# Kernel optimization log

Measured on AMD Instinct MI355X. Metric: run time of the kernel, lower is better.

## Reference

```python
import jax, jax.numpy as jnp
import numpy as np

B, S, D, H, DH = 2, 2048, 2048, 16, 128


def _rope(t, cos, sin):
    # t: [b,s,h,dh]; pairs are consecutive elements (view(..., -1, 2) in torch)
    te = t[..., 0::2]
    to = t[..., 1::2]
    re = te * cos - to * sin
    im = te * sin + to * cos
    return jnp.stack([re, im], axis=-1).reshape(t.shape)


def setup_inputs() -> dict:
    key = jax.random.key(0)
    ks = jax.random.split(key, 5)
    inv = 1.0 / np.sqrt(D)
    x = jax.random.normal(ks[0], (B, S, D), dtype=jnp.float32)
    # standard RoPE angle table -> cos/sin of shape [1,S,1,DH//2]
    pos = jnp.arange(S, dtype=jnp.float32)[:, None]
    freqs = 1.0 / (10000.0 ** (jnp.arange(0, DH, 2, dtype=jnp.float32) / DH))
    ang = pos * freqs[None, :]
    rope_cos = jnp.cos(ang)[None, :, None, :]
    rope_sin = jnp.sin(ang)[None, :, None, :]
    Wq = jax.random.normal(ks[1], (D, D), dtype=jnp.float32) * inv
    Wk = jax.random.normal(ks[2], (D, D), dtype=jnp.float32) * inv
    Wv = jax.random.normal(ks[3], (D, D), dtype=jnp.float32) * inv
    Wo = jax.random.normal(ks[4], (D, D), dtype=jnp.float32) * inv
    return {"x": x, "rope_cos": rope_cos, "rope_sin": rope_sin,
            "Wq": Wq, "Wk": Wk, "Wv": Wv, "Wo": Wo}


def reference(x, rope_cos, rope_sin, Wq, Wk, Wv, Wo):
    b, s, d = x.shape
    scale = DH ** (-0.5)
    # nn.Linear(bias=False): y = x @ W.T
    q = (x @ Wq.T).reshape(b, s, H, DH)
    k = (x @ Wk.T).reshape(b, s, H, DH)
    v = (x @ Wv.T).reshape(b, s, H, DH)
    q = _rope(q, rope_cos[:, :s], rope_sin[:, :s])
    k = _rope(k, rope_cos[:, :s], rope_sin[:, :s])
    q = q.transpose(0, 2, 1, 3)  # bhsd
    k = k.transpose(0, 2, 1, 3)
    v = v.transpose(0, 2, 1, 3)
    # full scores needed for softmax normalizer
    scores = jnp.einsum('bhqd,bhkd->bhqk', q, k) * scale
    lse = jax.nn.logsumexp(scores, axis=-1)  # [b,h,s]
    # torch.einsum('bhss,bhsd->bhsd', softmax(scores), v) takes the DIAGONAL
    # of the softmax matrix and scales v elementwise. Replicate exactly:
    diag = jnp.einsum('bhsd,bhsd->bhs', q, k) * scale  # scores[b,h,s,s]
    w = jnp.exp(diag - lse)  # softmax(scores)[b,h,s,s]
    out = w[..., None] * v  # [b,h,s,dh]
    out = out.transpose(0, 2, 1, 3).reshape(b, s, d)
    return out @ Wo.T
```

## Files before the change

kernel.cpp:

```cpp
#include <hip/hip_runtime.h>

#define B_  2
#define S_  2048
#define D_  2048
#define H_  16
#define DH_ 128
#define M_  (B_ * S_)

typedef __bf16 bf16;
typedef __bf16 bf16x2 __attribute__((ext_vector_type(2)));
typedef __bf16 bf16x4 __attribute__((ext_vector_type(4)));
typedef __bf16 bf16x8 __attribute__((ext_vector_type(8)));
typedef float  f32x4  __attribute__((ext_vector_type(4)));

static constexpr float kScale = 0.08838834764831845f;

__device__ __forceinline__ void async16(const void* g, void* l) {
  __builtin_amdgcn_global_load_lds(
      (const __attribute__((address_space(1))) void*)g,
      (__attribute__((address_space(3))) void*)l, 16, 0, 0);
}

__global__ void cvt_bf16(const float* __restrict__ s, bf16* __restrict__ d) {
  int i = (blockIdx.x * 256 + threadIdx.x) * 4;
  float4 v = *(const float4*)(s + i);
  bf16x4 o = {(bf16)v.x, (bf16)v.y, (bf16)v.z, (bf16)v.w};
  *(bf16x4*)(d + i) = o;
}

__global__ __launch_bounds__(256, 2) void gemm_qkv(
    const bf16* __restrict__ A, const bf16* __restrict__ Bm,
    bf16* __restrict__ qb, bf16* __restrict__ kb, bf16* __restrict__ vb) {
  __shared__ alignas(16) bf16 As[128 * 32];
  __shared__ alignas(16) bf16 Bs[128 * 32];
  const int tid = threadIdx.x;
  const int lane = tid & 63, wv = tid >> 6;
  const int quad = lane >> 4, c16 = lane & 15;
  const int wm = (wv >> 1) * 64, wn = (wv & 1) * 64;
  const int m0 = blockIdx.y * 128, n0 = blockIdx.x * 128;

  const bf16* ag = A  + (size_t)(m0 + (tid >> 2)) * D_ + (tid & 3) * 8;
  const bf16* bg = Bm + (size_t)(n0 + (tid >> 2)) * D_ + (tid & 3) * 8;
  char* asl = (char*)As + tid * 16;
  char* bsl = (char*)Bs + tid * 16;

  f32x4 acc[4][4] = {};
  for (int k0 = 0; k0 < D_; k0 += 32) {
    __syncthreads();
    async16(ag + k0,            asl);
    async16(ag + k0 + 64 * D_,  asl + 4096);
    async16(bg + k0,            bsl);
    async16(bg + k0 + 64 * D_,  bsl + 4096);
    __syncthreads();
    bf16x8 af[4], bfr[4];
#pragma unroll
    for (int i = 0; i < 4; ++i)
      af[i] = *(const bf16x8*)(As + (wm + i * 16 + c16) * 32 + quad * 8);
#pragma unroll
    for (int j = 0; j < 4; ++j)
      bfr[j] = *(const bf16x8*)(Bs + (wn + j * 16 + c16) * 32 + quad * 8);
#pragma unroll
    for (int i = 0; i < 4; ++i)
#pragma unroll
      for (int j = 0; j < 4; ++j)
        acc[i][j] = __builtin_amdgcn_mfma_f32_16x16x32_bf16(af[i], bfr[j], acc[i][j], 0, 0, 0);
  }

#pragma unroll
  for (int i = 0; i < 4; ++i)
#pragma unroll
    for (int j = 0; j < 4; ++j)
#pragma unroll
      for (int r = 0; r < 4; ++r) {
        int gm = m0 + wm + i * 16 + quad * 4 + r;
        int gn = n0 + wn + j * 16 + c16;
        float v = acc[i][j][r];
        int b = gm >> 11, s = gm & 2047;
        if (gn < 2048) {
          int h = gn >> 7, d = gn & 127;
          qb[(size_t)((b * 16 + h) * 2048 + s) * 128 + d] = (bf16)v;
        } else if (gn < 4096) {
          int h = (gn - 2048) >> 7, d = gn & 127;
          kb[(size_t)((b * 16 + h) * 2048 + s) * 128 + d] = (bf16)v;
        } else {
          vb[(size_t)gm * 2048 + (gn - 4096)] = (bf16)v;
        }
      }
}

__global__ void rope_kernel(bf16* __restrict__ q, bf16* __restrict__ k,
                            const float* __restrict__ cb, const float* __restrict__ sb) {
  int p  = blockIdx.x * 256 + threadIdx.x;
  int si = p & (S_ * 64 - 1);
  float c = cb[si], sn = sb[si];
  bf16x2* qp = (bf16x2*)q + p;
  bf16x2 qv = *qp;
  float te = (float)qv[0], to = (float)qv[1];
  bf16x2 oq = {(bf16)((te * c - to * sn) * kScale), (bf16)((te * sn + to * c) * kScale)};
  *qp = oq;
  bf16x2* kp = (bf16x2*)k + p;
  bf16x2 kv = *kp;
  te = (float)kv[0]; to = (float)kv[1];
  bf16x2 ok = {(bf16)(te * c - to * sn), (bf16)(te * sn + to * c)};
  *kp = ok;
}

__global__ __launch_bounds__(256, 2) void score_lse(
    const bf16* __restrict__ qb, const bf16* __restrict__ kb,
    float* __restrict__ lse, float* __restrict__ diag) {
  __shared__ alignas(16) bf16 Qs[4 * 128 * 32];
  __shared__ alignas(16) bf16 Ks[4 * 128 * 32];
  const int tid = threadIdx.x;
  const int lane = tid & 63, wv = tid >> 6;
  const int quad = lane >> 4, c16 = lane & 15;
  const int wm = wv * 32;
  const int bh = blockIdx.y;
  const int m0 = blockIdx.x * 128;
  const bf16* Q  = qb + (size_t)bh * (S_ * DH_);
  const bf16* Kp = kb + (size_t)bh * (S_ * DH_);

  const bf16* qg = Q + (size_t)(m0 + (tid >> 2)) * DH_ + (tid & 3) * 8;
  char* ql = (char*)Qs + tid * 16;
#pragma unroll
  for (int kt = 0; kt < 4; ++kt) {
    async16(qg + kt * 32,             ql + kt * 8192);
    async16(qg + kt * 32 + 64 * DH_,  ql + kt * 8192 + 4096);
  }

  const bf16* kg = Kp + (size_t)(tid >> 2) * DH_ + (tid & 3) * 8;
  char* kl = (char*)Ks + tid * 16;

  float sums[8] = {0.f, 0.f, 0.f, 0.f, 0.f, 0.f, 0.f, 0.f};

  for (int n0 = 0; n0 < S_; n0 += 128) {
    __syncthreads();
#pragma unroll
    for (int kt = 0; kt < 4; ++kt) {
      async16(kg + (size_t)n0 * DH_ + kt * 32,            kl + kt * 8192);
      async16(kg + (size_t)(n0 + 64) * DH_ + kt * 32,     kl + kt * 8192 + 4096);
    }
    __syncthreads();
    f32x4 acc[2][8] = {};
#pragma unroll
    for (int kt = 0; kt < 4; ++kt) {
      bf16x8 a[2], b[8];
#pragma unroll
      for (int i = 0; i < 2; ++i)
        a[i] = *(const bf16x8*)(Qs + kt * 4096 + (wm + i * 16 + c16) * 32 + quad * 8);
#pragma unroll
      for (int j = 0; j < 8; ++j)
        b[j] = *(const bf16x8*)(Ks + kt * 4096 + (j * 16 + c16) * 32 + quad * 8);
#pragma unroll
      for (int i = 0; i < 2; ++i)
#pragma unroll
        for (int j = 0; j < 8; ++j)
          acc[i][j] = __builtin_amdgcn_mfma_f32_16x16x32_bf16(a[i], b[j], acc[i][j], 0, 0, 0);
    }
#pragma unroll
    for (int i = 0; i < 2; ++i)
#pragma unroll
      for (int j = 0; j < 8; ++j)
#pragma unroll
        for (int r = 0; r < 4; ++r) {
          float sc = acc[i][j][r];
          int row = wm + i * 16 + quad * 4 + r;
          int col = j * 16 + c16;
          sums[i * 4 + r] += __expf(sc);
          if (n0 + col == m0 + row)
            diag[bh * S_ + m0 + row] = sc;
        }
  }

#pragma unroll
  for (int t = 0; t < 8; ++t) {
    float s = sums[t];
    s += __shfl_xor(s, 1);
    s += __shfl_xor(s, 2);
    s += __shfl_xor(s, 4);
    s += __shfl_xor(s, 8);
    if (c16 == 0) {
      int i = t >> 2, r = t & 3;
      lse[bh * S_ + m0 + wm + i * 16 + quad * 4 + r] = __logf(s);
    }
  }
}

__global__ void wv_mul(const bf16* __restrict__ vb, const float* __restrict__ lse,
                       const float* __restrict__ diag, bf16* __restrict__ t) {
  int u = blockIdx.x * 256 + threadIdx.x;
  int e = u * 8;
  int m = e >> 11;
  int c = e & 2047;
  int g = ((m >> 11) * 16 + (c >> 7)) * 2048 + (m & 2047);
  float w = __expf(diag[g] - lse[g]);
  bf16x8 v = ((const bf16x8*)vb)[u];
  bf16x8 o;
#pragma unroll
  for (int r = 0; r < 8; ++r) o[r] = (bf16)((float)v[r] * w);
  ((bf16x8*)t)[u] = o;
}

__global__ __launch_bounds__(256, 2) void gemm_out(
    const bf16* __restrict__ A, const bf16* __restrict__ Bm, float* __restrict__ C) {
  __shared__ alignas(16) bf16 As[128 * 32];
  __shared__ alignas(16) bf16 Bs[128 * 32];
  const int tid = threadIdx.x;
  const int lane = tid & 63, wv = tid >> 6;
  const int quad = lane >> 4, c16 = lane & 15;
  const int wm = (wv >> 1) * 64, wn = (wv & 1) * 64;
  const int m0 = blockIdx.y * 128, n0 = blockIdx.x * 128;

  const bf16* ag = A  + (size_t)(m0 + (tid >> 2)) * D_ + (tid & 3) * 8;
  const bf16* bg = Bm + (size_t)(n0 + (tid >> 2)) * D_ + (tid & 3) * 8;
  char* asl = (char*)As + tid * 16;
  char* bsl = (char*)Bs + tid * 16;

  f32x4 acc[4][4] = {};
  for (int k0 = 0; k0 < D_; k0 += 32) {
    __syncthreads();
    async16(ag + k0,            asl);
    async16(ag + k0 + 64 * D_,  asl + 4096);
    async16(bg + k0,            bsl);
    async16(bg + k0 + 64 * D_,  bsl + 4096);
    __syncthreads();
    bf16x8 af[4], bfr[4];
#pragma unroll
    for (int i = 0; i < 4; ++i)
      af[i] = *(const bf16x8*)(As + (wm + i * 16 + c16) * 32 + quad * 8);
#pragma unroll
    for (int j = 0; j < 4; ++j)
      bfr[j] = *(const bf16x8*)(Bs + (wn + j * 16 + c16) * 32 + quad * 8);
#pragma unroll
    for (int i = 0; i < 4; ++i)
#pragma unroll
      for (int j = 0; j < 4; ++j)
        acc[i][j] = __builtin_amdgcn_mfma_f32_16x16x32_bf16(af[i], bfr[j], acc[i][j], 0, 0, 0);
  }
#pragma unroll
  for (int i = 0; i < 4; ++i)
#pragma unroll
    for (int j = 0; j < 4; ++j)
#pragma unroll
      for (int r = 0; r < 4; ++r) {
        int gm = m0 + wm + i * 16 + quad * 4 + r;
        int gn = n0 + wn + j * 16 + c16;
        C[(size_t)gm * D_ + gn] = acc[i][j][r];
      }
}

extern "C" void kernel_launch(void* const* d_in, const int* in_sizes, int n_in,
                              void* d_out, int out_size, void* d_ws, size_t ws_size,
                              hipStream_t stream) {
  (void)in_sizes; (void)n_in; (void)out_size; (void)ws_size;
  const float* x  = (const float*)d_in[0];
  const float* rc = (const float*)d_in[1];
  const float* rs = (const float*)d_in[2];
  const float* Wq = (const float*)d_in[3];
  const float* Wk = (const float*)d_in[4];
  const float* Wv = (const float*)d_in[5];
  const float* Wo = (const float*)d_in[6];

  char* ws = (char*)d_ws;
  bf16* xb   = (bf16*)ws;
  bf16* wqkv = (bf16*)(ws + 16777216);
  bf16* wob  = (bf16*)(ws + 16777216 + 25165824);
  bf16* qb   = (bf16*)(ws + 16777216 + 25165824 + 8388608);
  bf16* kb   = qb + 8388608;
  bf16* vb   = kb + 8388608;
  float* lse = (float*)(vb + 8388608);
  float* dia = lse + 65536;

  cvt_bf16<<<8192, 256, 0, stream>>>(x,  xb);
  cvt_bf16<<<4096, 256, 0, stream>>>(Wq, wqkv);
  cvt_bf16<<<4096, 256, 0, stream>>>(Wk, wqkv + 4194304);
  cvt_bf16<<<4096, 256, 0, stream>>>(Wv, wqkv + 8388608);
  cvt_bf16<<<4096, 256, 0, stream>>>(Wo, wob);

  gemm_qkv<<<dim3(48, 32), 256, 0, stream>>>(xb, wqkv, qb, kb, vb);
  rope_kernel<<<16384, 256, 0, stream>>>(qb, kb, rc, rs);
  score_lse<<<dim3(16, 32), 256, 0, stream>>>(qb, kb, lse, dia);
  wv_mul<<<4096, 256, 0, stream>>>(vb, lse, dia, xb );
  gemm_out<<<dim3(16, 32), 256, 0, stream>>>(xb, wob, (float*)d_out);
}
```

Before: 396.2 us.

## Fuse RoPE into QKV GEMM epilogue and switch softmax to exp2

Removes the separate RoPE kernel by applying the rotation in the QKV GEMM epilogue, using lane shuffles to pair adjacent columns and writing bf16x2 stores. Folds log2(e) into the Q scale so the score kernel can use hardware exp2/log2. Diagonal extraction now runs only on the diagonal tile, and the output GEMM writes float2 stores. The cost is extra cos/sin loads and shuffles in the GEMM epilogue, plus slightly different rounding because RoPE is applied to the fp32 accumulator.

```diff
diff --git a/kernel.cpp b/kernel.cpp
--- a/kernel.cpp
+++ b/kernel.cpp
@@ -13,7 +13,10 @@
 typedef __bf16 bf16x8 __attribute__((ext_vector_type(8)));
 typedef float  f32x4  __attribute__((ext_vector_type(4)));
 
-static constexpr float kScale = 0.08838834764831845f;
+#define EXP2F(x) __builtin_amdgcn_exp2f(x)
+#define LOG2F(x) __builtin_amdgcn_logf(x)
+
+static constexpr float kQScale = 0.08838834764831845f * 1.4426950408889634f;
 
 __device__ __forceinline__ void async16(const void* g, void* l) {
   __builtin_amdgcn_global_load_lds(
@@ -30,6 +33,7 @@
 
 __global__ __launch_bounds__(256, 2) void gemm_qkv(
     const bf16* __restrict__ A, const bf16* __restrict__ Bm,
+    const float* __restrict__ rc, const float* __restrict__ rs,
     bf16* __restrict__ qb, bf16* __restrict__ kb, bf16* __restrict__ vb) {
   __shared__ alignas(16) bf16 As[128 * 32];
   __shared__ alignas(16) bf16 Bs[128 * 32];
@@ -66,43 +70,53 @@
         acc[i][j] = __builtin_amdgcn_mfma_f32_16x16x32_bf16(af[i], bfr[j], acc[i][j], 0, 0, 0);
   }
 
-#pragma unroll
-  for (int i = 0; i < 4; ++i)
-#pragma unroll
-    for (int j = 0; j < 4; ++j)
-#pragma unroll
-      for (int r = 0; r < 4; ++r) {
-        int gm = m0 + wm + i * 16 + quad * 4 + r;
-        int gn = n0 + wn + j * 16 + c16;
-        float v = acc[i][j][r];
-        int b = gm >> 11, s = gm & 2047;
-        if (gn < 2048) {
-          int h = gn >> 7, d = gn & 127;
-          qb[(size_t)((b * 16 + h) * 2048 + s) * 128 + d] = (bf16)v;
-        } else if (gn < 4096) {
-          int h = (gn - 2048) >> 7, d = gn & 127;
-          kb[(size_t)((b * 16 + h) * 2048 + s) * 128 + d] = (bf16)v;
-        } else {
-          vb[(size_t)gm * 2048 + (gn - 4096)] = (bf16)v;
+  if (n0 < 4096) {
+    bf16* dst = (n0 < 2048) ? qb : kb;
+    const float sc = (n0 < 2048) ? kQScale : 1.0f;
+#pragma unroll
+    for (int i = 0; i < 4; ++i) {
+      const int gmi = m0 + wm + i * 16 + quad * 4;
+#pragma unroll
+      for (int j = 0; j < 4; ++j) {
+        const int gn = n0 + wn + j * 16 + c16;
+        const int h = (gn >> 7) & 15;
+        const int d = gn & 127;
+#pragma unroll
+        for (int r = 0; r < 4; ++r) {
+          float v = acc[i][j][r];
+          float p = __shfl_xor(v, 1);
+          const int gm = gmi + r;
+          const int b = gm >> 11, s = gm & 2047;
+          const int si = s * 64 + (d >> 1);
+          float c = rc[si], sn = rs[si];
+          float re = (v * c - p * sn) * sc;
+          float im = (v * sn + p * c) * sc;
+          if (!(lane & 1)) {
+            bf16x2 o = {(bf16)re, (bf16)im};
+            *(bf16x2*)(dst + ((size_t)((b * 16 + h) * 2048 + s) * 128 + d)) = o;
+          }
         }
       }
-}
-
-__global__ void rope_kernel(bf16* __restrict__ q, bf16* __restrict__ k,
-                            const float* __restrict__ cb, const float* __restrict__ sb) {
-  int p  = blockIdx.x * 256 + threadIdx.x;
-  int si = p & (S_ * 64 - 1);
-  float c = cb[si], sn = sb[si];
-  bf16x2* qp = (bf16x2*)q + p;
-  bf16x2 qv = *qp;
-  float te = (float)qv[0], to = (float)qv[1];
-  bf16x2 oq = {(bf16)((te * c - to * sn) * kScale), (bf16)((te * sn + to * c) * kScale)};
-  *qp = oq;
-  bf16x2* kp = (bf16x2*)k + p;
-  bf16x2 kv = *kp;
-  te = (float)kv[0]; to = (float)kv[1];
-  bf16x2 ok = {(bf16)(te * c - to * sn), (bf16)(te * sn + to * c)};
-  *kp = ok;
+    }
+  } else {
+#pragma unroll
+    for (int i = 0; i < 4; ++i) {
+      const int gmi = m0 + wm + i * 16 + quad * 4;
+#pragma unroll
+      for (int j = 0; j < 4; ++j) {
+        const int gn = n0 + wn + j * 16 + c16 - 4096;
+#pragma unroll
+        for (int r = 0; r < 4; ++r) {
+          float v = acc[i][j][r];
+          float p = __shfl_xor(v, 1);
+          if (!(lane & 1)) {
+            bf16x2 o = {(bf16)v, (bf16)p};
+            *(bf16x2*)(vb + (size_t)(gmi + r) * 2048 + gn) = o;
+          }
+        }
+      }
+    }
+  }
 }
 
 __global__ __launch_bounds__(256, 2) void score_lse(
@@ -156,19 +170,24 @@
         for (int j = 0; j < 8; ++j)
           acc[i][j] = __builtin_amdgcn_mfma_f32_16x16x32_bf16(a[i], b[j], acc[i][j], 0, 0, 0);
     }
+    if (n0 == m0) {
+#pragma unroll
+      for (int i = 0; i < 2; ++i)
+#pragma unroll
+        for (int r = 0; r < 4; ++r) {
+          if (c16 == quad * 4 + r) {
+            int row = wm + i * 16 + quad * 4 + r;
+            diag[bh * S_ + m0 + row] = acc[i][2 * wv + i][r];
+          }
+        }
+    }
 #pragma unroll
     for (int i = 0; i < 2; ++i)
 #pragma unroll
       for (int j = 0; j < 8; ++j)
 #pragma unroll
-        for (int r = 0; r < 4; ++r) {
-          float sc = acc[i][j][r];
-          int row = wm + i * 16 + quad * 4 + r;
-          int col = j * 16 + c16;
-          sums[i * 4 + r] += __expf(sc);
-          if (n0 + col == m0 + row)
-            diag[bh * S_ + m0 + row] = sc;
-        }
+        for (int r = 0; r < 4; ++r)
+          sums[i * 4 + r] += EXP2F(acc[i][j][r]);
   }
 
 #pragma unroll
@@ -180,7 +199,7 @@
     s += __shfl_xor(s, 8);
     if (c16 == 0) {
       int i = t >> 2, r = t & 3;
-      lse[bh * S_ + m0 + wm + i * 16 + quad * 4 + r] = __logf(s);
+      lse[bh * S_ + m0 + wm + i * 16 + quad * 4 + r] = LOG2F(s);
     }
   }
 }
@@ -192,7 +211,7 @@
   int m = e >> 11;
   int c = e & 2047;
   int g = ((m >> 11) * 16 + (c >> 7)) * 2048 + (m & 2047);
-  float w = __expf(diag[g] - lse[g]);
+  float w = EXP2F(diag[g] - lse[g]);
   bf16x8 v = ((const bf16x8*)vb)[u];
   bf16x8 o;
 #pragma unroll
@@ -242,9 +261,14 @@
     for (int j = 0; j < 4; ++j)
 #pragma unroll
       for (int r = 0; r < 4; ++r) {
-        int gm = m0 + wm + i * 16 + quad * 4 + r;
-        int gn = n0 + wn + j * 16 + c16;
-        C[(size_t)gm * D_ + gn] = acc[i][j][r];
+        float v = acc[i][j][r];
+        float p = __shfl_xor(v, 1);
+        if (!(lane & 1)) {
+          int gm = m0 + wm + i * 16 + quad * 4 + r;
+          int gn = n0 + wn + j * 16 + c16;
+          float2 o = {v, p};
+          *(float2*)(C + (size_t)gm * D_ + gn) = o;
+        }
       }
 }
 
@@ -276,8 +300,7 @@
   cvt_bf16<<<4096, 256, 0, stream>>>(Wv, wqkv + 8388608);
   cvt_bf16<<<4096, 256, 0, stream>>>(Wo, wob);
 
-  gemm_qkv<<<dim3(48, 32), 256, 0, stream>>>(xb, wqkv, qb, kb, vb);
-  rope_kernel<<<16384, 256, 0, stream>>>(qb, kb, rc, rs);
+  gemm_qkv<<<dim3(48, 32), 256, 0, stream>>>(xb, wqkv, rc, rs, qb, kb, vb);
   score_lse<<<dim3(16, 32), 256, 0, stream>>>(qb, kb, lse, dia);
   wv_mul<<<4096, 256, 0, stream>>>(vb, lse, dia, xb );
   gemm_out<<<dim3(16, 32), 256, 0, stream>>>(xb, wob, (float*)d_out);
```

Result: slower. 691.0 us (+74.4%).
